# Kernel tuning notes

Hardware: AMD Instinct MI355X
Metric: run time of the kernel (lower is better)

## Reference

```python
import jax, jax.numpy as jnp
import numpy as np

N_HEADS = 16
D_MODEL = 1024


def setup_inputs() -> dict:
    key = jax.random.key(0)
    ks = jax.random.split(key, 9)
    B, S, D = 2, 2048, D_MODEL
    dk = D // N_HEADS
    std = 0.02
    return {
        "X": jax.random.normal(ks[0], (B, S, D), dtype=jnp.float32),
        "WQ": jax.random.normal(ks[1], (D, D), dtype=jnp.float32) * std,
        "bQ": jnp.zeros((D,), dtype=jnp.float32),
        "WK": jax.random.normal(ks[2], (D, D), dtype=jnp.float32) * std,
        "bK": jnp.zeros((D,), dtype=jnp.float32),
        "WV": jax.random.normal(ks[3], (D, D), dtype=jnp.float32) * std,
        "bV": jnp.zeros((D,), dtype=jnp.float32),
        "Wp": jax.random.normal(ks[4], (dk, dk), dtype=jnp.float32) * std,
        "bp": jnp.zeros((dk,), dtype=jnp.float32),
    }


def reference(X, WQ, bQ, WK, bK, WV, bV, Wp, bp):
    B, S, D = X.shape
    H = N_HEADS
    dk = D // H
    # QKV projections, split heads: [B, S, H, dk]
    q = (X @ WQ + bQ).reshape(B, S, H, dk)
    k = (X @ WK + bK).reshape(B, S, H, dk)
    v = (X @ WV + bV).reshape(B, S, H, dk)
    # scaled dot-product attention (mask path is identity in the source)
    scores = jnp.einsum("bqhd,bkhd->bhqk", q, k) / jnp.sqrt(jnp.float32(dk))
    attn = jax.nn.softmax(scores, axis=-1)  # [B, H, S, S]
    out = jnp.einsum("bhqk,bkhd->bqhd", attn, v)  # [B, S, H, dk]
    # per-head output projection (d_k -> d_k), then merge heads
    out = out @ Wp + bp
    return out.reshape(B, S, D)
```

## Files before the change

kernel.cpp:

```cpp
#include <hip/hip_runtime.h>
#include <hip/hip_bf16.h>

#define BATCH 2
#define SEQ   2048
#define DM    1024
#define NH    16
#define DKH   64

typedef __attribute__((ext_vector_type(8))) short bf16x8;
typedef __attribute__((ext_vector_type(4))) float f32x4;
typedef __attribute__((ext_vector_type(4))) unsigned short u16x4;

typedef __attribute__((address_space(1))) const unsigned int gu32;
typedef __attribute__((address_space(3))) unsigned int lu32;

#if __has_builtin(__builtin_amdgcn_exp2f)
#define EXP2(x) __builtin_amdgcn_exp2f(x)
#else
#define EXP2(x) exp2f(x)
#endif

__device__ __forceinline__ unsigned short bf16rne(float f) {
  unsigned u = __float_as_uint(f);
  u += 0x7FFFu + ((u >> 16) & 1u);
  return (unsigned short)(u >> 16);
}

__device__ __forceinline__ short f2bf(float f) {
  union { __hip_bfloat16 h; short s; } u;
  u.h = __float2bfloat16(f);
  return u.s;
}

__device__ __forceinline__ void gload_lds16(const void* g, void* l) {
  __builtin_amdgcn_global_load_lds((gu32*)g, (lu32*)l, 16, 0, 0);
}

__global__ __launch_bounds__(256) void cvt_x(const float* __restrict__ X,
                                             unsigned short* __restrict__ Xb) {
  int i0 = blockIdx.x * 256 + threadIdx.x;
#pragma unroll
  for (int p = 0; p < 4; ++p) {
    int i = i0 + p * (1024 * 256);
    f32x4 v = ((const f32x4*)X)[i];
    u16x4 o;
#pragma unroll
    for (int j = 0; j < 4; ++j) o[j] = bf16rne(v[j]);
    ((u16x4*)Xb)[i] = o;
  }
}

__global__ __launch_bounds__(256) void cvt_w(const float* __restrict__ WQ,
                                             const float* __restrict__ WK,
                                             const float* __restrict__ WV,
                                             unsigned short* __restrict__ Wt) {
  __shared__ float tile[64][65];
  const int id = blockIdx.x;
  const int k0 = (id & 15) * 64;
  const int n0 = (id >> 4) * 64;
  const float* W = (n0 < 1024) ? WQ : (n0 < 2048 ? WK : WV);
  const int nloc = n0 & 1023;
  const int t = threadIdx.x;
#pragma unroll
  for (int p = 0; p < 4; ++p) {
    const int idx = t + p * 256;
    const int kr = idx >> 4, f4 = (idx & 15) * 4;
    const f32x4 v = *(const f32x4*)(W + (size_t)(k0 + kr) * 1024 + nloc + f4);
    tile[kr][f4 + 0] = v[0]; tile[kr][f4 + 1] = v[1];
    tile[kr][f4 + 2] = v[2]; tile[kr][f4 + 3] = v[3];
  }
  __syncthreads();
#pragma unroll
  for (int p = 0; p < 4; ++p) {
    const int idx = t + p * 256;
    const int nr = idx >> 4, kc = (idx & 15) * 4;
    u16x4 o;
#pragma unroll
    for (int u = 0; u < 4; ++u) o[u] = bf16rne(tile[kc + u][nr]);
    *(u16x4*)(Wt + (size_t)(n0 + nr) * 1024 + k0 + kc) = o;
  }
}

__global__ __launch_bounds__(256) void gemm_qkv(
    const unsigned short* __restrict__ Xb, const unsigned short* __restrict__ Wt,
    const float* __restrict__ bQ, const float* __restrict__ bK, const float* __restrict__ bV,
    unsigned short* __restrict__ Qb, unsigned short* __restrict__ Kb,
    unsigned short* __restrict__ Vt) {
  __shared__ unsigned short lds[2][8192];
  const int id = blockIdx.x;
  const int xcd = id & 7, s = id >> 3;
  const int m0 = (xcd * 4 + (s & 3)) * 128;
  const int n0 = (s >> 2) * 128;
  const int t = threadIdx.x, lane = t & 63, w = t >> 6;
  const int g = lane >> 4, q16 = lane & 15;
  const int wr = w >> 1, wc = w & 1;

  f32x4 acc[4][4] = {};

  auto stage = [&](int buf, int kt) {
    const int k0 = kt * 32;
#pragma unroll
    for (int p = 0; p < 2; ++p) {
      const int ch = t + p * 256;
      const int row = ch >> 2, c = (ch & 3) * 8;
      gload_lds16(Xb + (size_t)(m0 + row) * DM + k0 + c,
                  &lds[buf][0] + (w * 64 + p * 256) * 8);
      gload_lds16(Wt + (size_t)(n0 + row) * DM + k0 + c,
                  &lds[buf][4096] + (w * 64 + p * 256) * 8);
    }
  };

  stage(0, 0);
  for (int kt = 0; kt < 32; ++kt) {
    __syncthreads();
    if (kt + 1 < 32) stage((kt + 1) & 1, kt + 1);
    const unsigned short* A = &lds[kt & 1][0];
    const unsigned short* B = &lds[kt & 1][4096];
    bf16x8 af[4], bfr[4];
#pragma unroll
    for (int mt = 0; mt < 4; ++mt)
      af[mt] = *(const bf16x8*)(A + (wr * 64 + mt * 16 + q16) * 32 + g * 8);
#pragma unroll
    for (int nt = 0; nt < 4; ++nt)
      bfr[nt] = *(const bf16x8*)(B + (wc * 64 + nt * 16 + q16) * 32 + g * 8);
#pragma unroll
    for (int mt = 0; mt < 4; ++mt)
#pragma unroll
      for (int nt = 0; nt < 4; ++nt)
        acc[mt][nt] = __builtin_amdgcn_mfma_f32_16x16x32_bf16(af[mt], bfr[nt], acc[mt][nt], 0, 0, 0);
  }

  const int rsel = n0 >> 10;
  const float* bias = rsel == 0 ? bQ : (rsel == 1 ? bK : bV);
  const float qscale = (rsel == 0) ? 0.125f * 1.4426950408889634f : 1.0f;
#pragma unroll
  for (int mt = 0; mt < 4; ++mt) {
#pragma unroll
    for (int nt = 0; nt < 4; ++nt) {
      const int col = n0 + wc * 64 + nt * 16 + q16;
      const int colin = col & 1023;
      const int row0 = m0 + wr * 64 + mt * 16 + g * 4;
      const float bv = bias[colin];
      if (rsel < 2) {
        unsigned short* dst = (rsel == 0 ? Qb : Kb);
#pragma unroll
        for (int r = 0; r < 4; ++r)
          dst[(size_t)(row0 + r) * DM + colin] = bf16rne((acc[mt][nt][r] + bv) * qscale);
      } else {
        u16x4 o;
#pragma unroll
        for (int r = 0; r < 4; ++r) o[r] = bf16rne(acc[mt][nt][r] + bv);
        *(u16x4*)(Vt + ((size_t)((row0 >> 11) * 1024 + colin)) * SEQ + (row0 & 2047)) = o;
      }
    }
  }
}

__global__ __launch_bounds__(512, 2) void attn_kernel(
    const unsigned short* __restrict__ Qb, const unsigned short* __restrict__ Kb,
    const unsigned short* __restrict__ Vt, const float* __restrict__ Wp,
    const float* __restrict__ bp, float* __restrict__ Out) {
  const int g0 = blockIdx.x;
  const int xcd = g0 & 7, s = g0 >> 3;
  const int bh = xcd * 4 + (s & 3);
  const int qb = s >> 2;
  const int b = bh >> 4, h = bh & 15;
  const int t = threadIdx.x, lane = t & 63, w = t >> 6;
  const int qw = w >> 1, ks = w & 1;
  const int g = lane >> 4, q16 = lane & 15;
  const int qbase = qb * 256 + qw * 64;

  __shared__ unsigned short kv[2][2][2][4096];

  bf16x8 Qf[4][2];
#pragma unroll
  for (int qt = 0; qt < 4; ++qt)
#pragma unroll
    for (int dh = 0; dh < 2; ++dh)
      Qf[qt][dh] = *(const bf16x8*)(Qb + (size_t)(b * SEQ + qbase + qt * 16 + q16) * DM +
                                    h * DKH + dh * 32 + g * 8);

  f32x4 accO[4][4] = {};
  float lrun[4] = {0.f, 0.f, 0.f, 0.f};

  const int koff = ((q16 >> 2) << 3) + (q16 & 3);
  const int swzr = ((q16 & 3) << 1) | ((q16 >> 2) & 1);
  const unsigned short* Kbase = Kb + (size_t)(b * SEQ) * DM + h * DKH;
  const unsigned short* Vbase = Vt + ((size_t)(b * 1024 + h * DKH)) * SEQ;

  auto stage = [&](int buf, int kb) {
    const int row = t >> 3, pc = t & 7;
    const int lc = pc ^ (((row & 3) << 1) | ((row >> 3) & 1));
#pragma unroll
    for (int ks2 = 0; ks2 < 2; ++ks2) {
      const int k0 = ks2 * 1024 + kb * 64;
      gload_lds16(Kbase + (size_t)(k0 + row) * DM + lc * 8,
                  (unsigned short*)&kv[buf][ks2][0][0] + t * 8);
      gload_lds16(Vbase + (size_t)row * SEQ + k0 + lc * 8,
                  (unsigned short*)&kv[buf][ks2][1][0] + t * 8);
    }
  };

  stage(0, 0);
  for (int kb = 0; kb < 16; ++kb) {
    __syncthreads();
    if (kb + 1 < 16) stage((kb + 1) & 1, kb + 1);
    const unsigned short* Kl = &kv[kb & 1][ks][0][0];
    const unsigned short* Vl = &kv[kb & 1][ks][1][0];
#pragma unroll
    for (int kk = 0; kk < 2; ++kk) {
      bf16x8 Kf[2][2], Vf[4];
#pragma unroll
      for (int ta = 0; ta < 2; ++ta)
#pragma unroll
        for (int dh = 0; dh < 2; ++dh) {
          const int r = kk * 32 + koff + ta * 4;
          Kf[ta][dh] = *(const bf16x8*)(Kl + (size_t)(r * 8 + ((dh * 4 + g) ^ swzr)) * 8);
        }
#pragma unroll
      for (int pt = 0; pt < 4; ++pt) {
        const int d = (pt >> 1) * 32 + koff + (pt & 1) * 4;
        Vf[pt] = *(const bf16x8*)(Vl + (size_t)(d * 8 + ((kk * 4 + g) ^ swzr)) * 8);
      }
#pragma unroll
      for (int qt = 0; qt < 4; ++qt) {
        f32x4 st0 = {}, st1 = {};
        st0 = __builtin_amdgcn_mfma_f32_16x16x32_bf16(Kf[0][0], Qf[qt][0], st0, 0, 0, 0);
        st0 = __builtin_amdgcn_mfma_f32_16x16x32_bf16(Kf[0][1], Qf[qt][1], st0, 0, 0, 0);
        st1 = __builtin_amdgcn_mfma_f32_16x16x32_bf16(Kf[1][0], Qf[qt][0], st1, 0, 0, 0);
        st1 = __builtin_amdgcn_mfma_f32_16x16x32_bf16(Kf[1][1], Qf[qt][1], st1, 0, 0, 0);
        float pv[8];
#pragma unroll
        for (int r = 0; r < 4; ++r) { pv[r] = EXP2(st0[r]); pv[4 + r] = EXP2(st1[r]); }
        lrun[qt] += ((pv[0] + pv[1]) + (pv[2] + pv[3])) + ((pv[4] + pv[5]) + (pv[6] + pv[7]));
        bf16x8 p8;
#pragma unroll
        for (int j = 0; j < 8; ++j) p8[j] = f2bf(pv[j]);
#pragma unroll
        for (int pt = 0; pt < 4; ++pt)
          accO[qt][pt] = __builtin_amdgcn_mfma_f32_16x16x32_bf16(Vf[pt], p8, accO[qt][pt], 0, 0, 0);
      }
    }
  }

  __syncthreads();
  float* ex = (float*)&kv[0][0][0][0] + (size_t)(qw * 64 + lane) * 36;
#define ST2(QA, QB)                                                     \
  {                                                                     \
    _Pragma("unroll") for (int pt = 0; pt < 4; ++pt) {                  \
      ((f32x4*)ex)[pt] = accO[QA][pt];                                  \
      ((f32x4*)ex)[4 + pt] = accO[QB][pt];                              \
    }                                                                   \
    ex[32] = lrun[QA]; ex[33] = lrun[QB];                               \
  }
#define LD2(QA, QB)                                                     \
  {                                                                     \
    _Pragma("unroll") for (int pt = 0; pt < 4; ++pt) {                  \
      accO[QA][pt] += ((f32x4*)ex)[pt];                                 \
      accO[QB][pt] += ((f32x4*)ex)[4 + pt];                             \
    }                                                                   \
    lrun[QA] += ex[32]; lrun[QB] += ex[33];                             \
  }
  if (ks == 1) ST2(0, 1)
  __syncthreads();
  if (ks == 0) { LD2(0, 1) ST2(2, 3) }
  __syncthreads();
  if (ks == 1) LD2(2, 3)
#undef ST2
#undef LD2

  bf16x8 wpf[4][2];
#pragma unroll
  for (int ft = 0; ft < 4; ++ft)
#pragma unroll
    for (int dh = 0; dh < 2; ++dh) {
      bf16x8 a;
#pragma unroll
      for (int j = 0; j < 8; ++j)
        a[j] = f2bf(Wp[(dh * 32 + g * 8 + j) * DKH + ft * 16 + q16]);
      wpf[ft][dh] = a;
    }

#define PROJ(QT)                                                                 \
  {                                                                              \
    float lr = lrun[QT];                                                         \
    lr += __shfl_xor(lr, 16, 64);                                                \
    lr += __shfl_xor(lr, 32, 64);                                                \
    const float rl = 1.0f / lr;                                                  \
    bf16x8 pd[2];                                                                \
    _Pragma("unroll") for (int dh = 0; dh < 2; ++dh) {                           \
      bf16x8 v;                                                                  \
      _Pragma("unroll") for (int r = 0; r < 4; ++r) {                            \
        v[r] = f2bf(accO[QT][dh * 2 + 0][r] * rl);                               \
        v[4 + r] = f2bf(accO[QT][dh * 2 + 1][r] * rl);                           \
      }                                                                          \
      pd[dh] = v;                                                                \
    }                                                                            \
    const int qg = qbase + QT * 16 + q16;                                        \
    _Pragma("unroll") for (int ft = 0; ft < 4; ++ft) {                           \
      f32x4 fo = {};                                                             \
      fo = __builtin_amdgcn_mfma_f32_16x16x32_bf16(wpf[ft][0], pd[0], fo, 0, 0, 0); \
      fo = __builtin_amdgcn_mfma_f32_16x16x32_bf16(wpf[ft][1], pd[1], fo, 0, 0, 0); \
      f32x4 o;                                                                   \
      _Pragma("unroll") for (int r = 0; r < 4; ++r)                              \
          o[r] = fo[r] + bp[ft * 16 + g * 4 + r];                                \
      *(f32x4*)(Out + (size_t)(b * SEQ + qg) * DM + h * DKH + ft * 16 + g * 4) = o; \
    }                                                                            \
  }
  if (ks == 0) { PROJ(0) PROJ(1) } else { PROJ(2) PROJ(3) }
#undef PROJ
}

extern "C" void kernel_launch(void* const* d_in, const int* in_sizes, int n_in,
                              void* d_out, int out_size, void* d_ws, size_t ws_size,
                              hipStream_t stream) {
  const float* X  = (const float*)d_in[0];
  const float* WQ = (const float*)d_in[1];
  const float* bQ = (const float*)d_in[2];
  const float* WK = (const float*)d_in[3];
  const float* bK = (const float*)d_in[4];
  const float* WV = (const float*)d_in[5];
  const float* bV = (const float*)d_in[6];
  const float* Wp = (const float*)d_in[7];
  const float* bp = (const float*)d_in[8];
  float* Out = (float*)d_out;

  char* ws = (char*)d_ws;
  unsigned short* Xb = (unsigned short*)(ws + 0);
  unsigned short* Wt = (unsigned short*)(ws + (size_t)(8  << 20));
  unsigned short* Qb = (unsigned short*)(ws + (size_t)(14 << 20));
  unsigned short* Kb = (unsigned short*)(ws + (size_t)(22 << 20));
  unsigned short* Vt = (unsigned short*)(ws + (size_t)(30 << 20));

  cvt_x<<<1024, 256, 0, stream>>>(X, Xb);
  cvt_w<<<768, 256, 0, stream>>>(WQ, WK, WV, Wt);
  gemm_qkv<<<768, 256, 0, stream>>>(Xb, Wt, bQ, bK, bV, Qb, Kb, Vt);
  attn_kernel<<<256, 512, 0, stream>>>(Qb, Kb, Vt, Wp, bp, Out);
}
```

Measured before the change: 89.70 us.

## Double attention block to 1024 threads with 32 query rows per wave

The attention kernel now runs 1024 threads per block: 16 waves, each handling 32 query rows instead of 64, while the block still covers 256 queries. The K/V staging is split so one half of the threads loads K and the other half loads V. The split-K reduction and the projection tail shrink to match. The aim is more waves in flight to hide the latency of the exp and shared-memory loads, at the cost of half as much Q reuse per wave and heavier block-wide syncs.

Measured after the change: 95.28 us. 1.06x slower.

```diff
diff --git a/kernel.cpp b/kernel.cpp
--- a/kernel.cpp
+++ b/kernel.cpp
@@ -156,32 +156,32 @@
   }
 }
 
-__global__ __launch_bounds__(512, 2) void attn_kernel(
+__global__ __launch_bounds__(1024, 1) void attn_kernel(
     const unsigned short* __restrict__ Qb, const unsigned short* __restrict__ Kb,
     const unsigned short* __restrict__ Vt, const float* __restrict__ Wp,
     const float* __restrict__ bp, float* __restrict__ Out) {
   const int g0 = blockIdx.x;
   const int xcd = g0 & 7, s = g0 >> 3;
   const int bh = xcd * 4 + (s & 3);
-  const int qb = s >> 2;
+  const int panel = s >> 2;
   const int b = bh >> 4, h = bh & 15;
   const int t = threadIdx.x, lane = t & 63, w = t >> 6;
   const int qw = w >> 1, ks = w & 1;
   const int g = lane >> 4, q16 = lane & 15;
-  const int qbase = qb * 256 + qw * 64;
+  const int qbase = panel * 256 + qw * 32;
 
   __shared__ unsigned short kv[2][2][2][4096];
 
-  bf16x8 Qf[4][2];
-#pragma unroll
-  for (int qt = 0; qt < 4; ++qt)
+  bf16x8 Qf[2][2];
+#pragma unroll
+  for (int qt = 0; qt < 2; ++qt)
 #pragma unroll
     for (int dh = 0; dh < 2; ++dh)
       Qf[qt][dh] = *(const bf16x8*)(Qb + (size_t)(b * SEQ + qbase + qt * 16 + q16) * DM +
                                     h * DKH + dh * 32 + g * 8);
 
-  f32x4 accO[4][4] = {};
-  float lrun[4] = {0.f, 0.f, 0.f, 0.f};
+  f32x4 accO[2][4] = {};
+  float lrun[2] = {0.f, 0.f};
 
   const int koff = ((q16 >> 2) << 3) + (q16 & 3);
   const int swzr = ((q16 & 3) << 1) | ((q16 >> 2) & 1);
@@ -189,15 +189,23 @@
   const unsigned short* Vbase = Vt + ((size_t)(b * 1024 + h * DKH)) * SEQ;
 
   auto stage = [&](int buf, int kb) {
-    const int row = t >> 3, pc = t & 7;
+    const int half = t >> 9, slot = t & 511;
+    const int row = slot >> 3, pc = slot & 7;
     const int lc = pc ^ (((row & 3) << 1) | ((row >> 3) & 1));
-#pragma unroll
-    for (int ks2 = 0; ks2 < 2; ++ks2) {
-      const int k0 = ks2 * 1024 + kb * 64;
-      gload_lds16(Kbase + (size_t)(k0 + row) * DM + lc * 8,
-                  (unsigned short*)&kv[buf][ks2][0][0] + t * 8);
-      gload_lds16(Vbase + (size_t)row * SEQ + k0 + lc * 8,
-                  (unsigned short*)&kv[buf][ks2][1][0] + t * 8);
+    if (half == 0) {
+#pragma unroll
+      for (int ks2 = 0; ks2 < 2; ++ks2) {
+        const int k0 = ks2 * 1024 + kb * 64;
+        gload_lds16(Kbase + (size_t)(k0 + row) * DM + lc * 8,
+                    (unsigned short*)&kv[buf][ks2][0][0] + slot * 8);
+      }
+    } else {
+#pragma unroll
+      for (int ks2 = 0; ks2 < 2; ++ks2) {
+        const int k0 = ks2 * 1024 + kb * 64;
+        gload_lds16(Vbase + (size_t)row * SEQ + k0 + lc * 8,
+                    (unsigned short*)&kv[buf][ks2][1][0] + slot * 8);
+      }
     }
   };
 
@@ -223,7 +231,7 @@
         Vf[pt] = *(const bf16x8*)(Vl + (size_t)(d * 8 + ((kk * 4 + g) ^ swzr)) * 8);
       }
 #pragma unroll
-      for (int qt = 0; qt < 4; ++qt) {
+      for (int qt = 0; qt < 2; ++qt) {
         f32x4 st0 = {}, st1 = {};
         st0 = __builtin_amdgcn_mfma_f32_16x16x32_bf16(Kf[0][0], Qf[qt][0], st0, 0, 0, 0);
         st0 = __builtin_amdgcn_mfma_f32_16x16x32_bf16(Kf[0][1], Qf[qt][1], st0, 0, 0, 0);
@@ -244,30 +252,28 @@
   }
 
   __syncthreads();
-  float* ex = (float*)&kv[0][0][0][0] + (size_t)(qw * 64 + lane) * 36;
-#define ST2(QA, QB)                                                     \
+  float* ex = (float*)&kv[0][0][0][0] + (size_t)(qw * 64 + lane) * 20;
+#define ST1(Q_)                                                         \
+  {                                                                     \
+    _Pragma("unroll") for (int pt = 0; pt < 4; ++pt)                    \
+        ((f32x4*)ex)[pt] = accO[Q_][pt];                                \
+    ex[16] = lrun[Q_];                                                  \
+  }
+#define LD1(Q_)                                                         \
   {                                                                     \
     _Pragma("unroll") for (int pt = 0; pt < 4; ++pt) {                  \
-      ((f32x4*)ex)[pt] = accO[QA][pt];                                  \
-      ((f32x4*)ex)[4 + pt] = accO[QB][pt];                              \
+      f32x4 v = ((f32x4*)ex)[pt];                                       \
+      _Pragma("unroll") for (int r = 0; r < 4; ++r) accO[Q_][pt][r] += v[r];\
     }                                                                   \
-    ex[32] = lrun[QA]; ex[33] = lrun[QB];                               \
-  }
-#define LD2(QA, QB)                                                     \
-  {                                                                     \
-    _Pragma("unroll") for (int pt = 0; pt < 4; ++pt) {                  \
-      accO[QA][pt] += ((f32x4*)ex)[pt];                                 \
-      accO[QB][pt] += ((f32x4*)ex)[4 + pt];                             \
-    }                                                                   \
-    lrun[QA] += ex[32]; lrun[QB] += ex[33];                             \
-  }
-  if (ks == 1) ST2(0, 1)
+    lrun[Q_] += ex[16];                                                 \
+  }
+  if (ks == 1) ST1(0)
   __syncthreads();
-  if (ks == 0) { LD2(0, 1) ST2(2, 3) }
+  if (ks == 0) { LD1(0) ST1(1) }
   __syncthreads();
-  if (ks == 1) LD2(2, 3)
-#undef ST2
-#undef LD2
+  if (ks == 1) LD1(1)
+#undef ST1
+#undef LD1
 
   bf16x8 wpf[4][2];
 #pragma unroll
@@ -307,7 +313,7 @@
       *(f32x4*)(Out + (size_t)(b * SEQ + qg) * DM + h * DKH + ft * 16 + g * 4) = o; \
     }                                                                            \
   }
-  if (ks == 0) { PROJ(0) PROJ(1) } else { PROJ(2) PROJ(3) }
+  if (ks == 0) PROJ(0) else PROJ(1)
 #undef PROJ
 }
 
@@ -335,5 +341,5 @@
   cvt_x<<<1024, 256, 0, stream>>>(X, Xb);
   cvt_w<<<768, 256, 0, stream>>>(WQ, WK, WV, Wt);
   gemm_qkv<<<768, 256, 0, stream>>>(Xb, Wt, bQ, bK, bV, Qb, Kb, Vt);
-  attn_kernel<<<256, 512, 0, stream>>>(Qb, Kb, Vt, Wp, bp, Out);
-}
+  attn_kernel<<<256, 1024, 0, stream>>>(Qb, Kb, Vt, Wp, bp, Out);
+}
```
